# Performance work log

Hardware: AMD Instinct MI355X
Metric: run time of the kernel (lower is better)

Reference implementation:

```python
import jax, jax.numpy as jnp
import numpy as np

B, Q, P, H, NH, NKV, D = 8, 16, 4096, 4096, 32, 8, 128
ROPE_BASE = 10000.0


def setup_inputs() -> dict:
    key = jax.random.key(0)
    ks = jax.random.split(key, 8)
    hidden_states = jax.random.normal(ks[0], (B, Q, H), dtype=jnp.float32)
    past_key = jax.random.normal(ks[1], (B, NKV, P, D), dtype=jnp.float32)
    past_value = jax.random.normal(ks[2], (B, NKV, P, D), dtype=jnp.float32)
    # draft tokens continue right after the cached prefix
    position_ids = jnp.broadcast_to(P + jnp.arange(Q, dtype=jnp.int64), (B, Q))
    attention_bias = jnp.zeros((B, 1, Q, P + Q), dtype=jnp.float32)
    s = 0.02
    Wq = jax.random.normal(ks[3], (H, NH * D), dtype=jnp.float32) * s
    Wk = jax.random.normal(ks[4], (H, NKV * D), dtype=jnp.float32) * s
    Wv = jax.random.normal(ks[5], (H, NKV * D), dtype=jnp.float32) * s
    Wo = jax.random.normal(ks[6], (NH * D, H), dtype=jnp.float32) * s
    return {"hidden_states": hidden_states, "position_ids": position_ids,
            "past_key": past_key, "past_value": past_value,
            "attention_bias": attention_bias, "Wq": Wq, "Wk": Wk, "Wv": Wv, "Wo": Wo}


def _rope_cos_sin(position_ids, dtype):
    # inv_freq over even dims, GPT-NeoX layout: angles repeated (concat) over halves
    inv_freq = 1.0 / (ROPE_BASE ** (jnp.arange(0, D, 2, dtype=jnp.float32) / D))
    ang = position_ids.astype(jnp.float32)[:, :, None] * inv_freq  # [B,Q,D/2]
    emb = jnp.concatenate([ang, ang], axis=-1)  # [B,Q,D]
    cos = jnp.cos(emb).astype(dtype)[:, None, :, :]  # [B,1,Q,D]
    sin = jnp.sin(emb).astype(dtype)[:, None, :, :]
    return cos, sin


def _rotate_half(x):
    x1, x2 = jnp.split(x, 2, axis=-1)
    return jnp.concatenate([-x2, x1], axis=-1)


def reference(hidden_states, position_ids, past_key, past_value, attention_bias,
              Wq, Wk, Wv, Wo):
    b, q_len, _ = hidden_states.shape
    n_kv = past_key.shape[1]
    groups = NH // n_kv
    # projections
    q = (hidden_states @ Wq).reshape(b, q_len, NH, D).transpose(0, 2, 1, 3)   # [B,NH,Q,D]
    k = (hidden_states @ Wk).reshape(b, q_len, n_kv, D).transpose(0, 2, 1, 3)  # [B,NKV,Q,D]
    v = (hidden_states @ Wv).reshape(b, q_len, n_kv, D).transpose(0, 2, 1, 3)
    # RoPE
    cos, sin = _rope_cos_sin(position_ids, hidden_states.dtype)
    q = q * cos + _rotate_half(q) * sin
    k = k * cos + _rotate_half(k) * sin
    # KV-cache append
    k_all = jnp.concatenate([past_key, k], axis=2)    # [B,NKV,S,D]
    v_all = jnp.concatenate([past_value, v], axis=2)
    # GQA attention: group query heads per kv head instead of repeat_interleave
    qg = q.reshape(b, n_kv, groups, q_len, D)
    scale = 1.0 / jnp.sqrt(jnp.asarray(D, dtype=hidden_states.dtype))
    scores = jnp.einsum('bkgqd,bksd->bkgqs', qg, k_all) * scale
    scores = scores + attention_bias[:, :, None, :, :]  # bias [B,1,Q,S] -> broadcast
    probs = jax.nn.softmax(scores, axis=-1)
    out = jnp.einsum('bkgqs,bksd->bkgqd', probs, v_all)  # [B,NKV,G,Q,D]
    out = out.reshape(b, NH, q_len, D).transpose(0, 2, 1, 3).reshape(b, q_len, NH * D)
    return out @ Wo
```

## Files before the change

kernel.cpp:

```cpp
#include <hip/hip_runtime.h>
#include <hip/hip_bf16.h>

#define NB 8
#define NQ 16
#define NP 4096
#define NHID 4096
#define NHEADS 32
#define NKVH 8
#define NG 4
#define ND 128
#define NM 128
#define NSEQ 4112
#define N_QKV 6144
#define SPLITK 8
#define NS 8

typedef __attribute__((ext_vector_type(8))) short bf16x8;
typedef __attribute__((ext_vector_type(4))) float f32x4;

__device__ __forceinline__ unsigned short f2bf(float f) {
  unsigned int u = __float_as_uint(f);
  u = (u + 0x7FFFu + ((u >> 16) & 1u)) >> 16;
  return (unsigned short)u;
}

__device__ __forceinline__ unsigned cvtpk(float lo, float hi) {
  unsigned r;
  asm("v_cvt_pk_bf16_f32 %0, %1, %2" : "=v"(r) : "v"(lo), "v"(hi));
  return r;
}

__device__ __forceinline__ float bf2f(unsigned short u) {
  return __uint_as_float(((unsigned)u) << 16);
}

#define TRREAD(dst, a32) \
  asm volatile("ds_read_b64_tr_b16 %0, %1" : "=v"(dst) : "v"(a32))
#define LGKM0() asm volatile("s_waitcnt lgkmcnt(0)" ::: "memory")
#define SBAR()                              \
  do {                                      \
    __builtin_amdgcn_sched_barrier(0);      \
    __builtin_amdgcn_s_barrier();           \
    __builtin_amdgcn_sched_barrier(0);      \
  } while (0)

__global__ __launch_bounds__(256) void k_cvt(const float* __restrict__ x,
                                             unsigned short* __restrict__ y, int n4) {
  int i = blockIdx.x * 256 + threadIdx.x;
  if (i >= n4) return;
  f32x4 v = ((const f32x4*)x)[i];
  uint2 o;
  o.x = cvtpk(v[0], v[1]);
  o.y = cvtpk(v[2], v[3]);
  ((uint2*)y)[i] = o;
}

template<int CT>
__global__ __launch_bounds__(256) void k_gemm(
    const unsigned short* __restrict__ A, int lda,
    const float* __restrict__ W0, const float* __restrict__ W1,
    const float* __restrict__ W2, int nw0, int nw1, int N, int KS,
    float* __restrict__ part) {
  constexpr int BN = CT * 32;
  constexpr int NT = CT * 2;
  constexpr int NW4 = BN / 4;
  constexpr int KST = 256 / NW4;
  __shared__ __align__(16) char Bl[8 * NT * 128];
  int n0 = blockIdx.x * BN;
  int k0 = blockIdx.y * KS;
  const float* Wp; int ldw, ncol;
  if (n0 < nw0)      { Wp = W0; ldw = nw0;       ncol = n0; }
  else if (n0 < nw1) { Wp = W1; ldw = nw1 - nw0; ncol = n0 - nw0; }
  else               { Wp = W2; ldw = N - nw1;   ncol = n0 - nw1; }
  int tid = threadIdx.x, lane = tid & 63, wid = tid >> 6;
  int r16 = lane & 15, hi = lane >> 4;
  int wr = wid >> 1, wc = wid & 1;
  int n4 = tid & (NW4 - 1), krow = tid / NW4;
  unsigned lb = (unsigned)(uintptr_t)(void*)Bl;

  f32x4 acc[4][CT];
#pragma unroll
  for (int i = 0; i < 4; ++i)
#pragma unroll
    for (int j = 0; j < CT; ++j) acc[i][j] = {0.f, 0.f, 0.f, 0.f};

  f32x4 cur[CT], nxt[CT];
#pragma unroll
  for (int r = 0; r < CT; ++r) {
    cur[r] = *(const f32x4*)&Wp[(size_t)(k0 + krow + r * KST) * ldw + ncol + n4 * 4];
    nxt[r] = cur[r];
  }

  for (int kk = 0; kk < KS; kk += 32) {
    SBAR();
    if (kk + 32 < KS) {
#pragma unroll
      for (int r = 0; r < CT; ++r)
        nxt[r] = *(const f32x4*)&Wp[(size_t)(k0 + kk + 32 + krow + r * KST) * ldw + ncol + n4 * 4];
    }
#pragma unroll
    for (int r = 0; r < CT; ++r) {
      int k = krow + r * KST;
      uint2 u;
      u.x = cvtpk(cur[r][0], cur[r][1]);
      u.y = cvtpk(cur[r][2], cur[r][3]);
      *(uint2*)(Bl + ((k >> 2) * NT + (n4 >> 2)) * 128 + (k & 3) * 32 + (n4 & 3) * 8) = u;
    }
    LGKM0();
    SBAR();
    bf16x8 af[4];
#pragma unroll
    for (int rt = 0; rt < 4; ++rt)
      af[rt] = *(const bf16x8*)&A[(size_t)(wr * 64 + rt * 16 + r16) * lda + k0 + kk + hi * 8];
    unsigned long long rr[2 * CT];
#pragma unroll
    for (int ct = 0; ct < CT; ++ct) {
      int s1 = hi * (2 * NT) + wc * CT + ct;
      TRREAD(rr[ct * 2],     lb + s1 * 128 + r16 * 8);
      TRREAD(rr[ct * 2 + 1], lb + (s1 + NT) * 128 + r16 * 8);
    }
    LGKM0();
    __builtin_amdgcn_sched_barrier(0);
    __builtin_amdgcn_s_setprio(1);
#pragma unroll
    for (int ct = 0; ct < CT; ++ct) {
      union { unsigned long long u[2]; bf16x8 v; } cc;
      cc.u[0] = rr[ct * 2]; cc.u[1] = rr[ct * 2 + 1];
#pragma unroll
      for (int rt = 0; rt < 4; ++rt)
        acc[rt][ct] = __builtin_amdgcn_mfma_f32_16x16x32_bf16(af[rt], cc.v, acc[rt][ct], 0, 0, 0);
    }
    __builtin_amdgcn_s_setprio(0);
#pragma unroll
    for (int r = 0; r < CT; ++r) cur[r] = nxt[r];
  }
  float* po = part + (size_t)blockIdx.y * NM * N;
#pragma unroll
  for (int rt = 0; rt < 4; ++rt)
#pragma unroll
    for (int ct = 0; ct < CT; ++ct)
#pragma unroll
      for (int r = 0; r < 4; ++r) {
        int m = wr * 64 + rt * 16 + hi * 4 + r;
        int n = n0 + wc * CT * 16 + ct * 16 + r16;
        po[(size_t)m * N + n] = acc[rt][ct][r];
      }
}

__global__ __launch_bounds__(256) void k_rope(
    const float* __restrict__ part, const void* __restrict__ posv,
    unsigned short* __restrict__ qb, unsigned short* __restrict__ kb,
    unsigned short* __restrict__ vb) {
  int t = blockIdx.x * 256 + threadIdx.x;
  int d = t & 63;
  int rest = t >> 6;
  int h = rest % 48;
  int m = rest / 48;
  if (m >= NM) return;
  const int* p32 = (const int*)posv;
  const long long* p64 = (const long long*)posv;
  bool is64 = (p64[0] == (long long)p32[0]);
  int pos = is64 ? (int)p64[m] : p32[m];
  int b = m >> 4, q = m & 15;

  int c1, c2;
  if (h < 32)      { c1 = h * ND + d; }
  else if (h < 40) { c1 = NHID + (h - 32) * ND + d; }
  else             { c1 = NHID + 1024 + (h - 40) * ND + d; }
  c2 = c1 + 64;
  float x1 = 0.f, x2 = 0.f;
#pragma unroll
  for (int c = 0; c < SPLITK; ++c) {
    x1 += part[((size_t)c * NM + m) * N_QKV + c1];
    x2 += part[((size_t)c * NM + m) * N_QKV + c2];
  }
  if (h < 40) {
    float invf = __expf(-(float)d * 0.14391156831212787f);
    float th = (float)pos * invf;
    float cs = cosf(th), sn = sinf(th);
    float o1 = x1 * cs - x2 * sn;
    float o2 = x2 * cs + x1 * sn;
    if (h < 32) {
      o1 *= 0.08838834764831845f;
      o2 *= 0.08838834764831845f;
      int kv = h >> 2, g = h & 3;
      size_t base = ((((size_t)b * NKVH + kv) * NG + g) * NQ + q) * ND;
      qb[base + d] = f2bf(o1);
      qb[base + d + 64] = f2bf(o2);
    } else {
      int kvh = h - 32;
      size_t base = (((size_t)b * NKVH + kvh) * NQ + q) * ND;
      kb[base + d] = f2bf(o1);
      kb[base + d + 64] = f2bf(o2);
    }
  } else {
    int kvh = h - 40;
    size_t base = (((size_t)b * NKVH + kvh) * NQ + q) * ND;
    vb[base + d] = f2bf(x1);
    vb[base + d + 64] = f2bf(x2);
  }
}

template<int NSPL>
__global__ __launch_bounds__(256, 2) void k_attn(
    const unsigned short* __restrict__ qb, const unsigned short* __restrict__ kb,
    const unsigned short* __restrict__ vb, const float* __restrict__ pastK,
    const float* __restrict__ pastV, const float* __restrict__ bias,
    unsigned short* __restrict__ pout, float* __restrict__ pml) {
  __shared__ __align__(16) char lds[81920];
  char* Pl = lds + 65536;
  constexpr int KEYS = NP / NSPL;
  constexpr int NSUB = KEYS / 64;
  int bkv = blockIdx.x;
  int split = blockIdx.y;
  int b = bkv >> 3, kv = bkv & 7;
  int tid = threadIdx.x, lane = tid & 63, wid = tid >> 6;
  int r16 = lane & 15, hi = lane >> 4;

  const unsigned short* qbase = qb + ((((size_t)b * NKVH + kv) * NG + wid) * NQ) * ND;
  bf16x8 qf[4];
#pragma unroll
  for (int kd = 0; kd < 4; ++kd)
    qf[kd] = *(const bf16x8*)&qbase[r16 * ND + kd * 32 + hi * 8];

  float m_run[4], l_lane[4];
  f32x4 oacc[8];
#pragma unroll
  for (int r = 0; r < 4; ++r) { m_run[r] = -1e30f; l_lane[r] = 0.f; }
#pragma unroll
  for (int dt = 0; dt < 8; ++dt) oacc[dt] = {0.f, 0.f, 0.f, 0.f};

  int s0 = split * KEYS;
  const float* Kg = pastK + ((size_t)(b * NKVH + kv) * NP + s0) * ND;
  const float* Vg = pastV + ((size_t)(b * NKVH + kv) * NP + s0) * ND;
  const float* biasrow = bias + (size_t)(b * NQ) * NSEQ;
  int d4 = tid & 31, sr = tid >> 5;
  bool last = (split == NSPL - 1);

  f32x4 rwK[8], rwV[8];
  float br[4], bt[4];
  bf16x8 tk, tv;

  auto kissue = [&](int tile) {
    const float* Kn = Kg + (size_t)tile * 64 * ND;
#pragma unroll
    for (int it = 0; it < 8; ++it)
      rwK[it] = *(const f32x4*)&Kn[(size_t)(sr + it * 8) * ND + d4 * 4];
  };
  auto vissue = [&](int tile) {
    const float* Vn = Vg + (size_t)tile * 64 * ND;
#pragma unroll
    for (int it = 0; it < 8; ++it)
      rwV[it] = *(const f32x4*)&Vn[(size_t)(sr + it * 8) * ND + d4 * 4];
  };
  auto bissue = [&](int tile) {
#pragma unroll
    for (int it = 0; it < 4; ++it) {
      int e = it * 256 + tid;
      int q = e >> 6, j = e & 63;
      br[it] = biasrow[(size_t)q * NSEQ + s0 + tile * 64 + j];
    }
  };
  auto kconv = [&](char* Kl) {
#pragma unroll
    for (int it = 0; it < 8; ++it) {
      int s = sr + it * 8;
      uint2 u;
      u.x = cvtpk(rwK[it][0], rwK[it][1]); u.y = cvtpk(rwK[it][2], rwK[it][3]);
      *(uint2*)(Kl + s * 256 + ((d4 * 8) ^ ((s & 7) << 4))) = u;
    }
  };
  auto vconv = [&](char* Vl) {
#pragma unroll
    for (int it = 0; it < 8; ++it) {
      int s = sr + it * 8;
      uint2 u;
      u.x = cvtpk(rwV[it][0], rwV[it][1]); u.y = cvtpk(rwV[it][2], rwV[it][3]);
      *(uint2*)(Vl + ((s >> 2) * 8 + (d4 >> 2)) * 128 + (s & 3) * 32 + (d4 & 3) * 8) = u;
    }
  };
  auto bstore = [&](char* Bb) {
#pragma unroll
    for (int it = 0; it < 4; ++it) {
      int e = it * 256 + tid;
      int q = e >> 6, j = e & 63;
      *(float*)(Bb + q * 256 + ((j * 4) ^ ((q & 7) << 4))) = br[it];
    }
  };

  f32x4 sc[4];
  auto qk_softmax = [&](char* Kl, char* Bb, bool tail) {
    __builtin_amdgcn_s_setprio(1);
#pragma unroll
    for (int ct = 0; ct < 4; ++ct) {
      f32x4 a = {0.f, 0.f, 0.f, 0.f};
      int s = ct * 16 + r16;
#pragma unroll
      for (int kd = 0; kd < 4; ++kd) {
        bf16x8 kf = *(const bf16x8*)(Kl + s * 256 + ((kd * 64 + hi * 16) ^ ((s & 7) << 4)));
        a = __builtin_amdgcn_mfma_f32_16x16x32_bf16(qf[kd], kf, a, 0, 0, 0);
      }
      sc[ct] = a;
    }
    __builtin_amdgcn_s_setprio(0);
    if (!tail) {
#pragma unroll
      for (int ct = 0; ct < 4; ++ct)
#pragma unroll
        for (int r = 0; r < 4; ++r) {
          int q = hi * 4 + r, j = ct * 16 + r16;
          sc[ct][r] += *(const float*)(Bb + q * 256 + ((j * 4) ^ ((q & 7) << 4)));
        }
    } else {
#pragma unroll
      for (int ct = 0; ct < 4; ++ct)
#pragma unroll
        for (int r = 0; r < 4; ++r) {
          if (ct == 0) sc[ct][r] += bt[r];
          else         sc[ct][r] = -1e30f;
        }
    }
    float pmax[4];
#pragma unroll
    for (int r = 0; r < 4; ++r)
      pmax[r] = fmaxf(fmaxf(sc[0][r], sc[1][r]), fmaxf(sc[2][r], sc[3][r]));
    bool ok = (pmax[0] <= m_run[0] + 8.f) && (pmax[1] <= m_run[1] + 8.f) &&
              (pmax[2] <= m_run[2] + 8.f) && (pmax[3] <= m_run[3] + 8.f);
    if (!__all(ok)) {
#pragma unroll
      for (int r = 0; r < 4; ++r) {
        float v = pmax[r];
        v = fmaxf(v, __shfl_xor(v, 1));
        v = fmaxf(v, __shfl_xor(v, 2));
        v = fmaxf(v, __shfl_xor(v, 4));
        v = fmaxf(v, __shfl_xor(v, 8));
        float mnew = fmaxf(m_run[r], v);
        float fac = __expf(m_run[r] - mnew);
        m_run[r] = mnew;
        l_lane[r] *= fac;
#pragma unroll
        for (int dt = 0; dt < 8; ++dt) oacc[dt][r] *= fac;
      }
    }
#pragma unroll
    for (int ct = 0; ct < 4; ++ct)
#pragma unroll
      for (int r = 0; r < 4; ++r) {
        float p = __expf(sc[ct][r] - m_run[r]);
        l_lane[r] += p;
        int q = hi * 4 + r, j = ct * 16 + r16;
        *(unsigned short*)(Pl + wid * 2048 + q * 128 + ((j * 2) ^ ((q & 7) << 4))) = f2bf(p);
      }
  };

  auto pv = [&](char* Vl) {
    unsigned vb32 = (unsigned)(uintptr_t)(void*)Vl;
#pragma unroll
    for (int kt = 0; kt < 2; ++kt) {
      bf16x8 pa = *(const bf16x8*)(Pl + wid * 2048 + r16 * 128 +
                                   ((kt * 64 + hi * 16) ^ ((r16 & 7) << 4)));
#pragma unroll
      for (int dh = 0; dh < 2; ++dh) {
        unsigned long long rr[8];
#pragma unroll
        for (int dq = 0; dq < 4; ++dq) {
          int sA = hi * 16 + kt * 64 + dh * 4 + dq;
          TRREAD(rr[dq * 2],     vb32 + sA * 128 + r16 * 8);
          TRREAD(rr[dq * 2 + 1], vb32 + (sA + 8) * 128 + r16 * 8);
        }
        LGKM0();
        __builtin_amdgcn_sched_barrier(0);
        __builtin_amdgcn_s_setprio(1);
#pragma unroll
        for (int dq = 0; dq < 4; ++dq) {
          union { unsigned long long u[2]; bf16x8 v; } cc;
          cc.u[0] = rr[dq * 2]; cc.u[1] = rr[dq * 2 + 1];
          oacc[dh * 4 + dq] = __builtin_amdgcn_mfma_f32_16x16x32_bf16(pa, cc.v, oacc[dh * 4 + dq], 0, 0, 0);
        }
        __builtin_amdgcn_s_setprio(0);
      }
    }
  };

  kissue(0);
  vissue(0);
  bissue(0);
  kconv(lds + 0);
  vconv(lds + 32768);
  bstore(lds + 73728);
  LGKM0();

  int cur = 0;
  for (int sub = 0; sub < NSUB; ++sub) {
    char* KlC = lds + cur * 16384;
    char* VlC = lds + 32768 + cur * 16384;
    char* BbC = lds + 73728 + cur * 4096;
    char* KlN = lds + (cur ^ 1) * 16384;
    char* VlN = lds + 32768 + (cur ^ 1) * 16384;
    char* BbN = lds + 73728 + (cur ^ 1) * 4096;
    SBAR();
    bool pf = (sub + 1 < NSUB);
    if (pf) {
      kissue(sub + 1);
      vissue(sub + 1);
      bissue(sub + 1);
    } else if (last) {
      int s = tid >> 4, d8 = tid & 15;
      const unsigned short* Kn = kb + (((size_t)b * NKVH + kv) * NQ) * ND;
      const unsigned short* Vn = vb + (((size_t)b * NKVH + kv) * NQ) * ND;
      tk = *(const bf16x8*)&Kn[s * ND + d8 * 8];
      tv = *(const bf16x8*)&Vn[s * ND + d8 * 8];
#pragma unroll
      for (int r = 0; r < 4; ++r)
        bt[r] = biasrow[(size_t)(hi * 4 + r) * NSEQ + NP + r16];
    }
    qk_softmax(KlC, BbC, false);
    if (pf) {
      kconv(KlN);
    } else if (last) {
      int s = tid >> 4, d8 = tid & 15;
      *(bf16x8*)(KlN + s * 256 + ((d8 * 16) ^ ((s & 7) << 4))) = tk;
    }
    pv(VlC);
    if (pf) {
      vconv(VlN);
      bstore(BbN);
    } else if (last) {
      int s = tid >> 4, d8 = tid & 15;
      *(bf16x8*)(VlN + ((s >> 2) * 8 + (d8 >> 1)) * 128 + (s & 3) * 32 + (d8 & 1) * 16) = tv;
    }
    LGKM0();
    if (pf || last) cur ^= 1;
  }
  if (last) {
    SBAR();
    qk_softmax(lds + cur * 16384, (char*)0, true);
    pv(lds + 32768 + cur * 16384);
  }

  float l_run[4];
#pragma unroll
  for (int r = 0; r < 4; ++r) {
    float s = l_lane[r];
    s += __shfl_xor(s, 1);
    s += __shfl_xor(s, 2);
    s += __shfl_xor(s, 4);
    s += __shfl_xor(s, 8);
    l_run[r] = s;
  }
  SBAR();
  char* My = lds + wid * 4096;
#pragma unroll
  for (int dt = 0; dt < 8; ++dt)
#pragma unroll
    for (int r = 0; r < 4; ++r)
      *(unsigned short*)(My + (hi * 4 + r) * 256 + (dt * 16 + r16) * 2) = f2bf(oacc[dt][r]);
  LGKM0();
  size_t rowbase = ((size_t)(b * NKVH + kv) * NG + wid) * NQ;
  unsigned short* po = pout + ((size_t)split * (NB * NKVH * NG * NQ) + rowbase) * ND;
#pragma unroll
  for (int it = 0; it < 4; ++it) {
    int row = it * 4 + (lane >> 4);
    uint4 vv = *(uint4*)(My + row * 256 + r16 * 16);
    *(uint4*)&po[(size_t)row * ND + r16 * 8] = vv;
  }
  if (r16 == 0) {
#pragma unroll
    for (int r = 0; r < 4; ++r) {
      size_t idx = ((size_t)split * (NB * NKVH * NG * NQ) + rowbase + hi * 4 + r) * 2;
      pml[idx] = m_run[r];
      pml[idx + 1] = l_run[r];
    }
  }
}

template<int NSPL>
__global__ __launch_bounds__(256) void k_combine(
    const unsigned short* __restrict__ pout, const float* __restrict__ pml,
    unsigned short* __restrict__ Aatt) {
  const int NROW = NB * NKVH * NG * NQ;
  int row = blockIdx.x * 2 + (threadIdx.x >> 7);
  int d = threadIdx.x & 127;
  float mv[NSPL], lv[NSPL];
  float M = -1e30f;
#pragma unroll
  for (int c = 0; c < NSPL; ++c) {
    mv[c] = pml[((size_t)c * NROW + row) * 2];
    lv[c] = pml[((size_t)c * NROW + row) * 2 + 1];
    M = fmaxf(M, mv[c]);
  }
  float L = 0.f, acc = 0.f;
#pragma unroll
  for (int c = 0; c < NSPL; ++c) {
    float w = __expf(mv[c] - M);
    L += lv[c] * w;
    acc += bf2f(pout[((size_t)c * NROW + row) * ND + d]) * w;
  }
  float o = acc / L;
  int q = row & 15, g = (row >> 4) & 3, kvh = (row >> 6) & 7, b = row >> 9;
  Aatt[(size_t)(b * NQ + q) * NHID + (kvh * NG + g) * ND + d] = f2bf(o);
}

__global__ __launch_bounds__(256) void k_red(const float* __restrict__ part,
                                             float* __restrict__ out) {
  int i = blockIdx.x * 256 + threadIdx.x;
  float s = 0.f;
#pragma unroll
  for (int c = 0; c < SPLITK; ++c) s += part[(size_t)c * (NM * NHID) + i];
  out[i] = s;
}

extern "C" void kernel_launch(void* const* d_in, const int* in_sizes, int n_in,
                              void* d_out, int out_size, void* d_ws, size_t ws_size,
                              hipStream_t stream) {
  const float* hidden = (const float*)d_in[0];
  const void* pos = d_in[1];
  const float* pastK = (const float*)d_in[2];
  const float* pastV = (const float*)d_in[3];
  const float* bias = (const float*)d_in[4];
  const float* Wq = (const float*)d_in[5];
  const float* Wk = (const float*)d_in[6];
  const float* Wv = (const float*)d_in[7];
  const float* Wo = (const float*)d_in[8];
  float* out = (float*)d_out;

  char* ws = (char*)d_ws;
  size_t off = 0;
  auto alloc = [&](size_t bytes) {
    char* p = ws + off;
    off += (bytes + 255) & ~(size_t)255;
    return p;
  };
  unsigned short* hb   = (unsigned short*)alloc((size_t)NM * NHID * 2);
  unsigned short* qb   = (unsigned short*)alloc((size_t)NB * NKVH * NG * NQ * ND * 2);
  unsigned short* kb   = (unsigned short*)alloc((size_t)NB * NKVH * NQ * ND * 2);
  unsigned short* vb   = (unsigned short*)alloc((size_t)NB * NKVH * NQ * ND * 2);
  unsigned short* Aatt = (unsigned short*)alloc((size_t)NM * NHID * 2);

  size_t mlB = (size_t)NS * 8192 * 2 * 4;
  float* pml = (float*)(ws + off);
  unsigned short* pout = (unsigned short*)(ws + off + mlB);
  float* part = (float*)(ws + off);

  k_cvt<<<512, 256, 0, stream>>>(hidden, hb, NM * NHID / 4);
  k_gemm<2><<<dim3(96, SPLITK), 256, 0, stream>>>(hb, NHID, Wq, Wk, Wv, 4096, 5120,
                                                  N_QKV, NHID / SPLITK, part);
  k_rope<<<1536, 256, 0, stream>>>(part, pos, qb, kb, vb);
  k_attn<NS><<<dim3(64, NS), 256, 0, stream>>>(qb, kb, vb, pastK, pastV, bias, pout, pml);
  k_combine<NS><<<4096, 256, 0, stream>>>(pout, pml, Aatt);
  k_gemm<2><<<dim3(64, SPLITK), 256, 0, stream>>>(Aatt, NHID, Wo, Wo, Wo, 4096, 8192,
                                                  NHID, NHID / SPLITK, part);
  k_red<<<2048, 256, 0, stream>>>(part, out);
}
```

Before: 154.0 us.

## Split each attention key tile across two wave halves with 512-thread blocks

The attention kernel now launches 512 threads (8 waves) per block. Each pair of waves serves the same query group but handles a different 32-key half of every 64-key tile, keeping its own online-softmax state. Each half writes a separate partial (m, l, O) slot, so the number of combine splits doubles. The V prefetch is also moved after the QK/softmax step. The aim is more memory-level parallelism and more waves to hide latency while streaming the fp32 KV cache. The cost is a larger combine pass, more partial-output traffic, and tighter per-thread register limits from the new launch bounds.

```diff
diff --git a/kernel.cpp b/kernel.cpp
--- a/kernel.cpp
+++ b/kernel.cpp
@@ -202,7 +202,7 @@
 }
 
 template<int NSPL>
-__global__ __launch_bounds__(256, 2) void k_attn(
+__global__ __launch_bounds__(512, 4) void k_attn(
     const unsigned short* __restrict__ qb, const unsigned short* __restrict__ kb,
     const unsigned short* __restrict__ vb, const float* __restrict__ pastK,
     const float* __restrict__ pastV, const float* __restrict__ bias,
@@ -216,8 +216,9 @@
   int b = bkv >> 3, kv = bkv & 7;
   int tid = threadIdx.x, lane = tid & 63, wid = tid >> 6;
   int r16 = lane & 15, hi = lane >> 4;
-
-  const unsigned short* qbase = qb + ((((size_t)b * NKVH + kv) * NG + wid) * NQ) * ND;
+  int g = wid & 3, half = wid >> 2;
+
+  const unsigned short* qbase = qb + ((((size_t)b * NKVH + kv) * NG + g) * NQ) * ND;
   bf16x8 qf[4];
 #pragma unroll
   for (int kd = 0; kd < 4; ++kd)
@@ -237,34 +238,36 @@
   int d4 = tid & 31, sr = tid >> 5;
   bool last = (split == NSPL - 1);
 
-  f32x4 rwK[8], rwV[8];
-  float br[4], bt[4];
+  f32x4 rwK[4], rwV[4];
+  float br0, br1, bt[4];
   bf16x8 tk, tv;
 
   auto kissue = [&](int tile) {
     const float* Kn = Kg + (size_t)tile * 64 * ND;
 #pragma unroll
-    for (int it = 0; it < 8; ++it)
-      rwK[it] = *(const f32x4*)&Kn[(size_t)(sr + it * 8) * ND + d4 * 4];
+    for (int it = 0; it < 4; ++it)
+      rwK[it] = *(const f32x4*)&Kn[(size_t)(sr + it * 16) * ND + d4 * 4];
   };
   auto vissue = [&](int tile) {
     const float* Vn = Vg + (size_t)tile * 64 * ND;
 #pragma unroll
-    for (int it = 0; it < 8; ++it)
-      rwV[it] = *(const f32x4*)&Vn[(size_t)(sr + it * 8) * ND + d4 * 4];
+    for (int it = 0; it < 4; ++it)
+      rwV[it] = *(const f32x4*)&Vn[(size_t)(sr + it * 16) * ND + d4 * 4];
   };
   auto bissue = [&](int tile) {
+    {
+      int e = tid;        int q = e >> 6, j = e & 63;
+      br0 = biasrow[(size_t)q * NSEQ + s0 + tile * 64 + j];
+    }
+    {
+      int e = 512 + tid;  int q = e >> 6, j = e & 63;
+      br1 = biasrow[(size_t)q * NSEQ + s0 + tile * 64 + j];
+    }
+  };
+  auto kconv = [&](char* Kl) {
 #pragma unroll
     for (int it = 0; it < 4; ++it) {
-      int e = it * 256 + tid;
-      int q = e >> 6, j = e & 63;
-      br[it] = biasrow[(size_t)q * NSEQ + s0 + tile * 64 + j];
-    }
-  };
-  auto kconv = [&](char* Kl) {
-#pragma unroll
-    for (int it = 0; it < 8; ++it) {
-      int s = sr + it * 8;
+      int s = sr + it * 16;
       uint2 u;
       u.x = cvtpk(rwK[it][0], rwK[it][1]); u.y = cvtpk(rwK[it][2], rwK[it][3]);
       *(uint2*)(Kl + s * 256 + ((d4 * 8) ^ ((s & 7) << 4))) = u;
@@ -272,29 +275,31 @@
   };
   auto vconv = [&](char* Vl) {
 #pragma unroll
-    for (int it = 0; it < 8; ++it) {
-      int s = sr + it * 8;
+    for (int it = 0; it < 4; ++it) {
+      int s = sr + it * 16;
       uint2 u;
       u.x = cvtpk(rwV[it][0], rwV[it][1]); u.y = cvtpk(rwV[it][2], rwV[it][3]);
       *(uint2*)(Vl + ((s >> 2) * 8 + (d4 >> 2)) * 128 + (s & 3) * 32 + (d4 & 3) * 8) = u;
     }
   };
   auto bstore = [&](char* Bb) {
-#pragma unroll
-    for (int it = 0; it < 4; ++it) {
-      int e = it * 256 + tid;
-      int q = e >> 6, j = e & 63;
-      *(float*)(Bb + q * 256 + ((j * 4) ^ ((q & 7) << 4))) = br[it];
-    }
-  };
-
-  f32x4 sc[4];
+    {
+      int e = tid;        int q = e >> 6, j = e & 63;
+      *(float*)(Bb + q * 256 + ((j * 4) ^ ((q & 7) << 4))) = br0;
+    }
+    {
+      int e = 512 + tid;  int q = e >> 6, j = e & 63;
+      *(float*)(Bb + q * 256 + ((j * 4) ^ ((q & 7) << 4))) = br1;
+    }
+  };
+
+  f32x4 sc[2];
   auto qk_softmax = [&](char* Kl, char* Bb, bool tail) {
     __builtin_amdgcn_s_setprio(1);
 #pragma unroll
-    for (int ct = 0; ct < 4; ++ct) {
+    for (int ct = 0; ct < 2; ++ct) {
       f32x4 a = {0.f, 0.f, 0.f, 0.f};
-      int s = ct * 16 + r16;
+      int s = half * 32 + ct * 16 + r16;
 #pragma unroll
       for (int kd = 0; kd < 4; ++kd) {
         bf16x8 kf = *(const bf16x8*)(Kl + s * 256 + ((kd * 64 + hi * 16) ^ ((s & 7) << 4)));
@@ -305,15 +310,15 @@
     __builtin_amdgcn_s_setprio(0);
     if (!tail) {
 #pragma unroll
-      for (int ct = 0; ct < 4; ++ct)
+      for (int ct = 0; ct < 2; ++ct)
 #pragma unroll
         for (int r = 0; r < 4; ++r) {
-          int q = hi * 4 + r, j = ct * 16 + r16;
+          int q = hi * 4 + r, j = half * 32 + ct * 16 + r16;
           sc[ct][r] += *(const float*)(Bb + q * 256 + ((j * 4) ^ ((q & 7) << 4)));
         }
     } else {
 #pragma unroll
-      for (int ct = 0; ct < 4; ++ct)
+      for (int ct = 0; ct < 2; ++ct)
 #pragma unroll
         for (int r = 0; r < 4; ++r) {
           if (ct == 0) sc[ct][r] += bt[r];
@@ -323,7 +328,7 @@
     float pmax[4];
 #pragma unroll
     for (int r = 0; r < 4; ++r)
-      pmax[r] = fmaxf(fmaxf(sc[0][r], sc[1][r]), fmaxf(sc[2][r], sc[3][r]));
+      pmax[r] = fmaxf(sc[0][r], sc[1][r]);
     bool ok = (pmax[0] <= m_run[0] + 8.f) && (pmax[1] <= m_run[1] + 8.f) &&
               (pmax[2] <= m_run[2] + 8.f) && (pmax[3] <= m_run[3] + 8.f);
     if (!__all(ok)) {
@@ -343,42 +348,39 @@
       }
     }
 #pragma unroll
-    for (int ct = 0; ct < 4; ++ct)
+    for (int ct = 0; ct < 2; ++ct)
 #pragma unroll
       for (int r = 0; r < 4; ++r) {
         float p = __expf(sc[ct][r] - m_run[r]);
         l_lane[r] += p;
-        int q = hi * 4 + r, j = ct * 16 + r16;
-        *(unsigned short*)(Pl + wid * 2048 + q * 128 + ((j * 2) ^ ((q & 7) << 4))) = f2bf(p);
+        int q = hi * 4 + r, j2 = ct * 16 + r16;
+        *(unsigned short*)(Pl + wid * 1024 + q * 64 + ((j2 * 2) ^ ((q & 3) << 4))) = f2bf(p);
       }
   };
 
   auto pv = [&](char* Vl) {
     unsigned vb32 = (unsigned)(uintptr_t)(void*)Vl;
-#pragma unroll
-    for (int kt = 0; kt < 2; ++kt) {
-      bf16x8 pa = *(const bf16x8*)(Pl + wid * 2048 + r16 * 128 +
-                                   ((kt * 64 + hi * 16) ^ ((r16 & 7) << 4)));
-#pragma unroll
-      for (int dh = 0; dh < 2; ++dh) {
-        unsigned long long rr[8];
-#pragma unroll
-        for (int dq = 0; dq < 4; ++dq) {
-          int sA = hi * 16 + kt * 64 + dh * 4 + dq;
-          TRREAD(rr[dq * 2],     vb32 + sA * 128 + r16 * 8);
-          TRREAD(rr[dq * 2 + 1], vb32 + (sA + 8) * 128 + r16 * 8);
-        }
-        LGKM0();
-        __builtin_amdgcn_sched_barrier(0);
-        __builtin_amdgcn_s_setprio(1);
-#pragma unroll
-        for (int dq = 0; dq < 4; ++dq) {
-          union { unsigned long long u[2]; bf16x8 v; } cc;
-          cc.u[0] = rr[dq * 2]; cc.u[1] = rr[dq * 2 + 1];
-          oacc[dh * 4 + dq] = __builtin_amdgcn_mfma_f32_16x16x32_bf16(pa, cc.v, oacc[dh * 4 + dq], 0, 0, 0);
-        }
-        __builtin_amdgcn_s_setprio(0);
-      }
+    bf16x8 pa = *(const bf16x8*)(Pl + wid * 1024 + r16 * 64 +
+                                 ((hi * 16) ^ ((r16 & 3) << 4)));
+#pragma unroll
+    for (int dh = 0; dh < 2; ++dh) {
+      unsigned long long rr[8];
+#pragma unroll
+      for (int dq = 0; dq < 4; ++dq) {
+        int sA = half * 64 + hi * 16 + dh * 4 + dq;
+        TRREAD(rr[dq * 2],     vb32 + sA * 128 + r16 * 8);
+        TRREAD(rr[dq * 2 + 1], vb32 + (sA + 8) * 128 + r16 * 8);
+      }
+      LGKM0();
+      __builtin_amdgcn_sched_barrier(0);
+      __builtin_amdgcn_s_setprio(1);
+#pragma unroll
+      for (int dq = 0; dq < 4; ++dq) {
+        union { unsigned long long u[2]; bf16x8 v; } cc;
+        cc.u[0] = rr[dq * 2]; cc.u[1] = rr[dq * 2 + 1];
+        oacc[dh * 4 + dq] = __builtin_amdgcn_mfma_f32_16x16x32_bf16(pa, cc.v, oacc[dh * 4 + dq], 0, 0, 0);
+      }
+      __builtin_amdgcn_s_setprio(0);
     }
   };
 
@@ -402,40 +404,50 @@
     bool pf = (sub + 1 < NSUB);
     if (pf) {
       kissue(sub + 1);
-      vissue(sub + 1);
       bissue(sub + 1);
     } else if (last) {
-      int s = tid >> 4, d8 = tid & 15;
-      const unsigned short* Kn = kb + (((size_t)b * NKVH + kv) * NQ) * ND;
-      const unsigned short* Vn = vb + (((size_t)b * NKVH + kv) * NQ) * ND;
-      tk = *(const bf16x8*)&Kn[s * ND + d8 * 8];
-      tv = *(const bf16x8*)&Vn[s * ND + d8 * 8];
-#pragma unroll
-      for (int r = 0; r < 4; ++r)
-        bt[r] = biasrow[(size_t)(hi * 4 + r) * NSEQ + NP + r16];
+      if (tid < 256) {
+        int s = tid >> 4, d8 = tid & 15;
+        const unsigned short* Kn = kb + (((size_t)b * NKVH + kv) * NQ) * ND;
+        const unsigned short* Vn = vb + (((size_t)b * NKVH + kv) * NQ) * ND;
+        tk = *(const bf16x8*)&Kn[s * ND + d8 * 8];
+        tv = *(const bf16x8*)&Vn[s * ND + d8 * 8];
+      }
+      if (half == 0) {
+#pragma unroll
+        for (int r = 0; r < 4; ++r)
+          bt[r] = biasrow[(size_t)(hi * 4 + r) * NSEQ + NP + r16];
+      }
     }
     qk_softmax(KlC, BbC, false);
     if (pf) {
       kconv(KlN);
+      vissue(sub + 1);
     } else if (last) {
-      int s = tid >> 4, d8 = tid & 15;
-      *(bf16x8*)(KlN + s * 256 + ((d8 * 16) ^ ((s & 7) << 4))) = tk;
+      if (tid < 256) {
+        int s = tid >> 4, d8 = tid & 15;
+        *(bf16x8*)(KlN + s * 256 + ((d8 * 16) ^ ((s & 7) << 4))) = tk;
+      }
     }
     pv(VlC);
     if (pf) {
       vconv(VlN);
       bstore(BbN);
     } else if (last) {
-      int s = tid >> 4, d8 = tid & 15;
-      *(bf16x8*)(VlN + ((s >> 2) * 8 + (d8 >> 1)) * 128 + (s & 3) * 32 + (d8 & 1) * 16) = tv;
+      if (tid < 256) {
+        int s = tid >> 4, d8 = tid & 15;
+        *(bf16x8*)(VlN + ((s >> 2) * 8 + (d8 >> 1)) * 128 + (s & 3) * 32 + (d8 & 1) * 16) = tv;
+      }
     }
     LGKM0();
     if (pf || last) cur ^= 1;
   }
   if (last) {
     SBAR();
-    qk_softmax(lds + cur * 16384, (char*)0, true);
-    pv(lds + 32768 + cur * 16384);
+    if (half == 0) {
+      qk_softmax(lds + cur * 16384, (char*)0, true);
+      pv(lds + 32768 + cur * 16384);
+    }
   }
 
   float l_run[4];
@@ -456,8 +468,10 @@
     for (int r = 0; r < 4; ++r)
       *(unsigned short*)(My + (hi * 4 + r) * 256 + (dt * 16 + r16) * 2) = f2bf(oacc[dt][r]);
   LGKM0();
-  size_t rowbase = ((size_t)(b * NKVH + kv) * NG + wid) * NQ;
-  unsigned short* po = pout + ((size_t)split * (NB * NKVH * NG * NQ) + rowbase) * ND;
+  const int NROW = NB * NKVH * NG * NQ;
+  int slot = split * 2 + half;
+  size_t rowbase = ((size_t)(b * NKVH + kv) * NG + g) * NQ;
+  unsigned short* po = pout + ((size_t)slot * NROW + rowbase) * ND;
 #pragma unroll
   for (int it = 0; it < 4; ++it) {
     int row = it * 4 + (lane >> 4);
@@ -467,7 +481,7 @@
   if (r16 == 0) {
 #pragma unroll
     for (int r = 0; r < 4; ++r) {
-      size_t idx = ((size_t)split * (NB * NKVH * NG * NQ) + rowbase + hi * 4 + r) * 2;
+      size_t idx = ((size_t)slot * NROW + rowbase + hi * 4 + r) * 2;
       pml[idx] = m_run[r];
       pml[idx + 1] = l_run[r];
     }
@@ -537,7 +551,7 @@
   unsigned short* vb   = (unsigned short*)alloc((size_t)NB * NKVH * NQ * ND * 2);
   unsigned short* Aatt = (unsigned short*)alloc((size_t)NM * NHID * 2);
 
-  size_t mlB = (size_t)NS * 8192 * 2 * 4;
+  size_t mlB = (size_t)(NS * 2) * 8192 * 2 * 4;
   float* pml = (float*)(ws + off);
   unsigned short* pout = (unsigned short*)(ws + off + mlB);
   float* part = (float*)(ws + off);
@@ -546,8 +560,8 @@
   k_gemm<2><<<dim3(96, SPLITK), 256, 0, stream>>>(hb, NHID, Wq, Wk, Wv, 4096, 5120,
                                                   N_QKV, NHID / SPLITK, part);
   k_rope<<<1536, 256, 0, stream>>>(part, pos, qb, kb, vb);
-  k_attn<NS><<<dim3(64, NS), 256, 0, stream>>>(qb, kb, vb, pastK, pastV, bias, pout, pml);
-  k_combine<NS><<<4096, 256, 0, stream>>>(pout, pml, Aatt);
+  k_attn<NS><<<dim3(64, NS), 512, 0, stream>>>(qb, kb, vb, pastK, pastV, bias, pout, pml);
+  k_combine<NS * 2><<<4096, 256, 0, stream>>>(pout, pml, Aatt);
   k_gemm<2><<<dim3(64, SPLITK), 256, 0, stream>>>(Aatt, NHID, Wo, Wo, Wo, 4096, 8192,
                                                   NHID, NHID / SPLITK, part);
   k_red<<<2048, 256, 0, stream>>>(part, out);
```

New measurement: 203.4 us. 1.32x slower.
